# Optimization experiments

Hardware: AMD Instinct MI355X
Metric: run time of the kernel (lower is better)

## Reference

```python
import jax, jax.numpy as jnp
import numpy as np

B, L, H = 32, 1024, 384


def setup_inputs() -> dict:
    key = jax.random.key(0)
    k1, k2 = jax.random.split(key)
    encoder_hidden_states = jax.random.normal(k1, (B, L, H), dtype=jnp.float32)
    durations_gt = jax.random.randint(k2, (B, L), 0, 8, dtype=jnp.int32)
    return {"encoder_hidden_states": encoder_hidden_states, "durations_gt": durations_gt}


def reference(encoder_hidden_states, durations_gt):
    # cumulative end-frame of each phoneme: [B, L]
    cum = jnp.cumsum(durations_gt, axis=1)
    total = cum[:, -1]                      # [B] expanded length per batch item
    T = int(jnp.max(total))                 # max expanded length (data-dependent)
    t = jnp.arange(T, dtype=cum.dtype)      # [T] output frame positions
    # source phoneme index for each output frame: number of cum entries <= t
    idx = jax.vmap(lambda c: jnp.searchsorted(c, t, side="right"))(cum)  # [B, T]
    idx = jnp.minimum(idx, L - 1)
    mask = (t[None, :] < total[:, None]).astype(jnp.float32)             # [B, T]
    # gather hidden states and zero out the padded tail
    out = jnp.take_along_axis(encoder_hidden_states, idx[:, :, None], axis=1)
    out = out * mask[:, :, None]
    return out, mask
```

## Files before the change

kernel.cpp:

```cpp
#include <hip/hip_runtime.h>

#define BB 32
#define LL 1024
#define HH 384
#define H4 (HH / 4)
#define TT 64
#define NT 256

__global__ __launch_bounds__(NT) void lenreg_kernel(
    const float* __restrict__ ehs,
    const int* __restrict__ dur,
    float* __restrict__ out,
    float* __restrict__ mask,
    int T)
{
    __shared__ int scum[LL];
    __shared__ int psum[NT];
    __shared__ int sidx[TT];

    const int tid = threadIdx.x;
    const int b   = blockIdx.y;
    const int t0  = blockIdx.x * TT;

    int4 d = ((const int4*)(dur + (size_t)b * LL))[tid];
    int p0 = d.x;
    int p1 = p0 + d.y;
    int p2 = p1 + d.z;
    int p3 = p2 + d.w;
    psum[tid] = p3;
    __syncthreads();
    #pragma unroll
    for (int off = 1; off < NT; off <<= 1) {
        int v = (tid >= off) ? psum[tid - off] : 0;
        __syncthreads();
        psum[tid] += v;
        __syncthreads();
    }
    const int excl = (tid > 0) ? psum[tid - 1] : 0;
    scum[4 * tid + 0] = excl + p0;
    scum[4 * tid + 1] = excl + p1;
    scum[4 * tid + 2] = excl + p2;
    scum[4 * tid + 3] = excl + p3;
    __syncthreads();

    const int total = scum[LL - 1];

    if (tid < TT) {
        const int t = t0 + tid;
        int lo = 0, hi = LL;
        while (lo < hi) {
            const int mid = (lo + hi) >> 1;
            if (scum[mid] <= t) lo = mid + 1; else hi = mid;
        }
        sidx[tid] = (lo < LL - 1) ? lo : (LL - 1);
        if (t < T) mask[(size_t)b * T + t] = (t < total) ? 1.0f : 0.0f;
    }
    __syncthreads();

    const float4* __restrict__ src_base = (const float4*)(ehs + (size_t)b * LL * HH);
    float4* __restrict__ out4 = (float4*)out;
    const float4 zero4 = make_float4(0.f, 0.f, 0.f, 0.f);

    for (int w = tid; w < TT * H4; w += NT) {
        const int tl = w / H4;
        const int v  = w - tl * H4;
        const int t  = t0 + tl;
        if (t >= T) break;
        float4 val = zero4;
        if (t < total) {
            val = src_base[(size_t)sidx[tl] * H4 + v];
        }
        out4[((size_t)b * T + t) * H4 + v] = val;
    }
}

extern "C" void kernel_launch(void* const* d_in, const int* in_sizes, int n_in,
                              void* d_out, int out_size, void* d_ws, size_t ws_size,
                              hipStream_t stream) {
    const float* ehs = (const float*)d_in[0];
    const int*   dur = (const int*)d_in[1];

    const int T = out_size / (BB * (HH + 1));

    float* out  = (float*)d_out;
    float* mask = (float*)d_out + (size_t)BB * T * HH;

    dim3 grid((T + TT - 1) / TT, BB);
    dim3 block(NT);
    lenreg_kernel<<<grid, block, 0, stream>>>(ehs, dur, out, mask, T);
}
```

Measured before the change: 229.2 us.

## Use wave shuffle scan, larger frame tiles, and nontemporal output stores

Replaces the shared-memory Hillis-Steele prefix sum with a wavefront shuffle scan plus a small cross-wave combine, which removes many block barriers. Doubles the frames per block so the per-block cumsum and setup are amortized over more output, and writes output and mask with nontemporal stores to avoid polluting cache. This halves the grid size, which may reduce occupancy or parallelism, and the nontemporal stores may or may not help on this hardware.

```diff
diff --git a/kernel.cpp b/kernel.cpp
--- a/kernel.cpp
+++ b/kernel.cpp
@@ -4,8 +4,10 @@
 #define LL 1024
 #define HH 384
 #define H4 (HH / 4)
-#define TT 64
+#define TT 128
 #define NT 256
+
+typedef float f32x4 __attribute__((ext_vector_type(4)));
 
 __global__ __launch_bounds__(NT) void lenreg_kernel(
     const float* __restrict__ ehs,
@@ -15,28 +17,35 @@
     int T)
 {
     __shared__ int scum[LL];
-    __shared__ int psum[NT];
+    __shared__ int wsum[4];
     __shared__ int sidx[TT];
 
-    const int tid = threadIdx.x;
-    const int b   = blockIdx.y;
-    const int t0  = blockIdx.x * TT;
+    const int tid  = threadIdx.x;
+    const int lane = tid & 63;
+    const int wav  = tid >> 6;
+    const int b    = blockIdx.y;
+    const int t0   = blockIdx.x * TT;
 
     int4 d = ((const int4*)(dur + (size_t)b * LL))[tid];
-    int p0 = d.x;
-    int p1 = p0 + d.y;
-    int p2 = p1 + d.z;
-    int p3 = p2 + d.w;
-    psum[tid] = p3;
+    const int p0 = d.x;
+    const int p1 = p0 + d.y;
+    const int p2 = p1 + d.z;
+    const int p3 = p2 + d.w;
+
+    int v = p3;
+    #pragma unroll
+    for (int off = 1; off < 64; off <<= 1) {
+        const int u = __shfl_up(v, off, 64);
+        if (lane >= off) v += u;
+    }
+    if (lane == 63) wsum[wav] = v;
     __syncthreads();
+    int woff = 0;
     #pragma unroll
-    for (int off = 1; off < NT; off <<= 1) {
-        int v = (tid >= off) ? psum[tid - off] : 0;
-        __syncthreads();
-        psum[tid] += v;
-        __syncthreads();
+    for (int i = 0; i < 3; ++i) {
+        if (i < wav) woff += wsum[i];
     }
-    const int excl = (tid > 0) ? psum[tid - 1] : 0;
+    const int excl = woff + v - p3;
     scum[4 * tid + 0] = excl + p0;
     scum[4 * tid + 1] = excl + p1;
     scum[4 * tid + 2] = excl + p2;
@@ -53,24 +62,27 @@
             if (scum[mid] <= t) lo = mid + 1; else hi = mid;
         }
         sidx[tid] = (lo < LL - 1) ? lo : (LL - 1);
-        if (t < T) mask[(size_t)b * T + t] = (t < total) ? 1.0f : 0.0f;
+        if (t < T) {
+            const float mv = (t < total) ? 1.0f : 0.0f;
+            __builtin_nontemporal_store(mv, mask + (size_t)b * T + t);
+        }
     }
     __syncthreads();
 
-    const float4* __restrict__ src_base = (const float4*)(ehs + (size_t)b * LL * HH);
-    float4* __restrict__ out4 = (float4*)out;
-    const float4 zero4 = make_float4(0.f, 0.f, 0.f, 0.f);
+    const f32x4* __restrict__ src_base = (const f32x4*)(ehs + (size_t)b * LL * HH);
+    f32x4* __restrict__ out4 = (f32x4*)out;
+    const f32x4 zero4 = (f32x4){0.f, 0.f, 0.f, 0.f};
 
     for (int w = tid; w < TT * H4; w += NT) {
         const int tl = w / H4;
-        const int v  = w - tl * H4;
+        const int vv = w - tl * H4;
         const int t  = t0 + tl;
         if (t >= T) break;
-        float4 val = zero4;
+        f32x4 val = zero4;
         if (t < total) {
-            val = src_base[(size_t)sidx[tl] * H4 + v];
+            val = src_base[(size_t)sidx[tl] * H4 + vv];
         }
-        out4[((size_t)b * T + t) * H4 + v] = val;
+        __builtin_nontemporal_store(val, &out4[((size_t)b * T + t) * H4 + vv]);
     }
 }
 
@@ -86,6 +98,5 @@
     float* mask = (float*)d_out + (size_t)BB * T * HH;
 
     dim3 grid((T + TT - 1) / TT, BB);
-    dim3 block(NT);
-    lenreg_kernel<<<grid, block, 0, stream>>>(ehs, dur, out, mask, T);
+    lenreg_kernel<<<grid, dim3(NT), 0, stream>>>(ehs, dur, out, mask, T);
 }
```

New measurement: 240.0 us. +4.7%, slower.
